# Optimization experiments

Hardware: AMD Instinct MI355X
Metric: run time of the kernel (lower is better)

The kernel has to match this reference:

```python
import jax, jax.numpy as jnp
import numpy as np

SELU_SCALE = 1.0507009873554805
SELU_ALPHA = 1.6732632423543772

def _learned_activation(x, w):
    # softmax-blended mixture of 8 activations plus a zero 'linear' branch
    p = jax.nn.softmax(w)
    sig = jax.nn.sigmoid(x)
    elu = jax.nn.elu(x)
    tanh = jnp.tanh(x)
    relu = jax.nn.relu(x)
    silu = jax.nn.silu(x)
    gelu = jax.nn.gelu(x, approximate=False)
    selu = SELU_SCALE * jnp.where(x > 0, x, SELU_ALPHA * jnp.expm1(x))
    mish = x * jnp.tanh(jax.nn.softplus(x))
    return (p[0] * sig + p[1] * elu + p[2] * tanh + p[3] * relu
            + p[4] * silu + p[5] * gelu + p[6] * selu + p[7] * mish)  # p[8]*0 (linear=0)


def setup_inputs() -> dict:
    key = jax.random.key(0)
    ks = jax.random.split(key, 10)
    B, D, H, E, M = 1024, 1024, 2048, 8, 2048
    init_units = 1024
    s = lambda fan_in: 1.0 / np.sqrt(fan_in)
    x = jax.random.normal(ks[0], (B, D), jnp.float32)
    gate_w = jax.random.normal(ks[1], (D, E), jnp.float32) * s(D)
    expert_w = jax.random.normal(ks[2], (E, D, H), jnp.float32) * s(D)
    expert_b = jnp.zeros((E, H), jnp.float32)
    conn_w1 = jax.random.normal(ks[3], (E, H, 32), jnp.float32) * s(H)
    conn_b1 = jnp.zeros((E, 32), jnp.float32)
    conn_w2 = jax.random.normal(ks[4], (E, 32, H), jnp.float32) * s(32)
    conn_b2 = jnp.zeros((E, H), jnp.float32)
    neuron_avg = jax.random.uniform(ks[5], (E, H), jnp.float32)
    # initial mask: first initial_units neurons active per expert
    neuron_mask = jnp.tile(
        jnp.concatenate([jnp.ones((init_units,), jnp.float32),
                         jnp.zeros((H - init_units,), jnp.float32)])[None, :], (E, 1))
    mem_read_w = jax.random.normal(ks[6], (H, M), jnp.float32) * s(H)
    mem_read_b = jnp.zeros((M,), jnp.float32)
    memory = jax.random.normal(ks[7], (M, H), jnp.float32) * s(M)
    act_w = jnp.ones((9,), jnp.float32)
    return {"x": x, "gate_w": gate_w, "expert_w": expert_w, "expert_b": expert_b,
            "conn_w1": conn_w1, "conn_b1": conn_b1, "conn_w2": conn_w2, "conn_b2": conn_b2,
            "neuron_avg": neuron_avg, "neuron_mask": neuron_mask,
            "mem_read_w": mem_read_w, "mem_read_b": mem_read_b,
            "memory": memory, "act_w": act_w}


def reference(x, gate_w, expert_w, expert_b, conn_w1, conn_b1, conn_w2, conn_b2,
              neuron_avg, neuron_mask, mem_read_w, mem_read_b, memory, act_w):
    # --- MoE gate over experts ---
    gate = jax.nn.softmax(x @ gate_w, axis=-1)  # [B, E]
    # --- DynamicConnectivity soft gating, per expert (from neuron_activation_avg) ---
    h1 = jax.nn.relu(jnp.einsum('eh,ehk->ek', neuron_avg, conn_w1) + conn_b1)  # [E, 32]
    conn = jax.nn.sigmoid(jnp.einsum('ek,ekh->eh', h1, conn_w2) + conn_b2)     # [E, H]
    # --- plastic dense experts: z -> gated -> masked -> relu ---
    z = jnp.einsum('bd,edh->ebh', x, expert_w) + expert_b[:, None, :]  # [E, B, H]
    a = jax.nn.relu(z * (conn * neuron_mask)[:, None, :])              # [E, B, H]
    moe_out = jnp.einsum('be,ebh->bh', gate, a)                        # [B, H]
    # --- episodic memory read (attention over memory slots) ---
    attn = jax.nn.softmax(moe_out @ mem_read_w + mem_read_b, axis=-1)  # [B, M]
    read_vec = attn @ memory                                           # [B, H]
    # --- blended learned activation on residual sum ---
    return _learned_activation(moe_out + read_vec, act_w)
```

## Files before the change

kernel.cpp:

```cpp
#include <hip/hip_runtime.h>
#include <hip/hip_bf16.h>
#include <math.h>

typedef __bf16 bf16_t;
typedef __bf16 bf16x8 __attribute__((ext_vector_type(8)));
typedef float f32x4 __attribute__((ext_vector_type(4)));

#define B_DIM 1024
#define D_DIM 1024
#define H_DIM 2048
#define E_DIM 8
#define M_DIM 2048

typedef const __attribute__((address_space(1))) unsigned int as1_uint;
typedef __attribute__((address_space(3))) unsigned int as3_uint;

__device__ __forceinline__ void gl_lds16(const void* g, void* l) {
  __builtin_amdgcn_global_load_lds((as1_uint*)g, (as3_uint*)l, 16, 0, 0);
}

__global__ __launch_bounds__(256) void cvt_kernel(const float* __restrict__ in,
                                                  bf16_t* __restrict__ out) {
  size_t i = ((size_t)blockIdx.x * 256 + threadIdx.x) * 8;
  float4 a = *(const float4*)&in[i];
  float4 b = *(const float4*)&in[i + 4];
  bf16x8 o;
  o[0] = (bf16_t)a.x; o[1] = (bf16_t)a.y; o[2] = (bf16_t)a.z; o[3] = (bf16_t)a.w;
  o[4] = (bf16_t)b.x; o[5] = (bf16_t)b.y; o[6] = (bf16_t)b.z; o[7] = (bf16_t)b.w;
  *(bf16x8*)&out[i] = o;
}

__global__ __launch_bounds__(256) void transpose_all(
    const float* __restrict__ ew, const float* __restrict__ mrw, const float* __restrict__ mem,
    bf16_t* __restrict__ wbT, bf16_t* __restrict__ mrT, bf16_t* __restrict__ memT) {
  __shared__ float tile[64][65];
  const int z = blockIdx.z;
  const float* in; bf16_t* out; int R, C;
  if (z < 8) {
    if (blockIdx.y >= 16) return;
    in = ew + (size_t)z * D_DIM * H_DIM; out = wbT + (size_t)z * D_DIM * H_DIM;
    R = D_DIM; C = H_DIM;
  } else if (z == 8) {
    in = mrw; out = mrT; R = H_DIM; C = M_DIM;
  } else {
    in = mem; out = memT; R = M_DIM; C = H_DIM;
  }
  int c0 = blockIdx.x * 64, r0 = blockIdx.y * 64;
  int t = threadIdx.x;
  int cq = (t & 15) * 4, rr = t >> 4;
#pragma unroll
  for (int i = 0; i < 4; ++i) {
    int r = rr + 16 * i;
    float4 v = *(const float4*)&in[(size_t)(r0 + r) * C + c0 + cq];
    tile[r][cq] = v.x; tile[r][cq + 1] = v.y; tile[r][cq + 2] = v.z; tile[r][cq + 3] = v.w;
  }
  __syncthreads();
  int r8 = (t & 7) * 8, cc = t >> 3;
#pragma unroll
  for (int i = 0; i < 2; ++i) {
    int c = cc + 32 * i;
    bf16x8 o;
#pragma unroll
    for (int j = 0; j < 8; ++j) o[j] = (bf16_t)tile[r8 + j][c];
    *(bf16x8*)&out[(size_t)(c0 + c) * R + r0 + r8] = o;
  }
}

__global__ __launch_bounds__(256) void gate_kernel(
    const float* __restrict__ x, const float* __restrict__ gw, float* __restrict__ gate_t) {
  __shared__ float red[256][8];
  int b = blockIdx.x, t = threadIdx.x;
  float acc[8] = {0.f, 0.f, 0.f, 0.f, 0.f, 0.f, 0.f, 0.f};
  for (int d = t; d < D_DIM; d += 256) {
    float xv = x[(size_t)b * D_DIM + d];
#pragma unroll
    for (int e = 0; e < 8; ++e) acc[e] += xv * gw[d * 8 + e];
  }
#pragma unroll
  for (int e = 0; e < 8; ++e) red[t][e] = acc[e];
  __syncthreads();
  for (int s = 128; s > 0; s >>= 1) {
    if (t < s) {
#pragma unroll
      for (int e = 0; e < 8; ++e) red[t][e] += red[t + s][e];
    }
    __syncthreads();
  }
  if (t == 0) {
    float m = red[0][0];
#pragma unroll
    for (int e = 1; e < 8; ++e) m = fmaxf(m, red[0][e]);
    float p[8], sum = 0.f;
#pragma unroll
    for (int e = 0; e < 8; ++e) { p[e] = expf(red[0][e] - m); sum += p[e]; }
    float inv = 1.f / sum;
#pragma unroll
    for (int e = 0; e < 8; ++e) gate_t[e * B_DIM + b] = p[e] * inv;
  }
}

__global__ __launch_bounds__(256) void conn1_kernel(
    const float* __restrict__ avg, const float* __restrict__ w1, float* __restrict__ h1p) {
  __shared__ float red[256 * 32];
  int e = blockIdx.x >> 3, c = blockIdx.x & 7, t = threadIdx.x;
  int h = c * 256 + t;
  float av = avg[e * H_DIM + h];
  const float* w1p = &w1[((size_t)e * H_DIM + h) * 32];
#pragma unroll
  for (int k = 0; k < 32; ++k) red[t * 32 + k] = av * w1p[k];
  __syncthreads();
  for (int s = 128; s > 0; s >>= 1) {
    if (t < s) {
#pragma unroll
      for (int k = 0; k < 32; ++k) red[t * 32 + k] += red[(t + s) * 32 + k];
    }
    __syncthreads();
  }
  if (t < 32) h1p[(e * 8 + c) * 32 + t] = red[t];
}

__global__ __launch_bounds__(256) void conn2_kernel(
    const float* __restrict__ h1p, const float* __restrict__ b1,
    const float* __restrict__ w2, const float* __restrict__ b2,
    const float* __restrict__ mask, float* __restrict__ conn) {
  __shared__ float h1[32];
  int e = blockIdx.x >> 3, c = blockIdx.x & 7, t = threadIdx.x;
  if (t < 32) {
    float s = 0.f;
#pragma unroll
    for (int c2 = 0; c2 < 8; ++c2) s += h1p[(e * 8 + c2) * 32 + t];
    h1[t] = fmaxf(s + b1[e * 32 + t], 0.f);
  }
  __syncthreads();
  int h = c * 256 + t;
  float s = b2[e * H_DIM + h];
#pragma unroll
  for (int k = 0; k < 32; ++k) s += h1[k] * w2[((size_t)e * 32 + k) * H_DIM + h];
  conn[e * H_DIM + h] = (1.f / (1.f + expf(-s))) * mask[e * H_DIM + h];
}

__global__ __launch_bounds__(512, 2) void expert_gemm(
    const bf16_t* __restrict__ A, const bf16_t* __restrict__ Bt,
    float* __restrict__ moe, bf16_t* __restrict__ moebf,
    const float* __restrict__ gate_t, const float* __restrict__ conn,
    const float* __restrict__ ebias) {
  __shared__ bf16_t As[2][128 * 64];
  __shared__ bf16_t Bs[8][64 * 64];

  const int wid = (blockIdx.x & 7) * 32 + (blockIdx.x >> 3);
  const int b0 = (wid & 7) * 128;
  const int n0 = (wid >> 3) * 64;

  const int t = threadIdx.x;
  const int lane = t & 63, wave = t >> 6;
  const int wmh = wave >> 2, wnq = wave & 3;
  const int lr = lane & 15, lk = (lane >> 4) * 8;
  const int csw = (lr & 7) << 3;
  const int srow = lane >> 3;
  const int scol = ((lane & 7) ^ srow) << 3;
  const size_t EB = (size_t)H_DIM * D_DIM;

  const bf16_t* Asrc = A + (size_t)(b0 + wave * 16 + srow) * D_DIM + scol;
  const bf16_t* Bsrc = Bt + (size_t)(n0 + wave * 8 + srow) * D_DIM + scol;

  auto stageA = [&](int buf, int kt) {
    gl_lds16(Asrc + (size_t)kt * 64, &As[buf][(wave * 16) * 64]);
    gl_lds16(Asrc + 8 * D_DIM + (size_t)kt * 64, &As[buf][(wave * 16 + 8) * 64]);
  };
  auto stageB = [&](int buf, int e, int kt) {
    gl_lds16(Bsrc + (size_t)e * EB + (size_t)kt * 64, &Bs[buf][(wave * 8) * 64]);
  };

  f32x4 acc[8][4];
#pragma unroll
  for (int e = 0; e < 8; ++e)
#pragma unroll
    for (int mf = 0; mf < 4; ++mf) acc[e][mf] = (f32x4){0.f, 0.f, 0.f, 0.f};

  stageA(0, 0);
#pragma unroll
  for (int s = 0; s < 5; ++s) stageB(s, s, 0);

  for (int kt = 0; kt < 16; ++kt) {
    const int ab = kt & 1;
    const bool nl = (kt < 15);
    bf16x8 af[2][4];
#pragma unroll
    for (int e = 0; e < 8; ++e) {
      if (e < 3) {
        stageB((e + 5) & 7, (e + 5) & 7, kt);
      } else if (nl) {
        stageB((e + 5) & 7, (e + 5) & 7, kt + 1);
        if (e == 3) stageA(ab ^ 1, kt + 1);
      }
      if (e < 3) {
        asm volatile("s_waitcnt vmcnt(5)" ::: "memory");
      } else if (nl) {
        asm volatile("s_waitcnt vmcnt(7)" ::: "memory");
      } else {
        if (e == 3) asm volatile("s_waitcnt vmcnt(4)" ::: "memory");
        if (e == 4) asm volatile("s_waitcnt vmcnt(3)" ::: "memory");
        if (e == 5) asm volatile("s_waitcnt vmcnt(2)" ::: "memory");
        if (e == 6) asm volatile("s_waitcnt vmcnt(1)" ::: "memory");
        if (e == 7) asm volatile("s_waitcnt vmcnt(0)" ::: "memory");
      }
      __builtin_amdgcn_s_barrier();
      __builtin_amdgcn_sched_barrier(0);
      if (e == 0) {
#pragma unroll
        for (int kk = 0; kk < 2; ++kk)
#pragma unroll
          for (int mf = 0; mf < 4; ++mf)
            af[kk][mf] = *(const bf16x8*)&As[ab][(wmh * 64 + mf * 16 + lr) * 64 +
                                                ((kk * 32 + lk) ^ csw)];
      }
      const bf16_t* Bb = &Bs[e][0];
      bf16x8 bf0 = *(const bf16x8*)&Bb[(wnq * 16 + lr) * 64 + (lk ^ csw)];
      bf16x8 bf1 = *(const bf16x8*)&Bb[(wnq * 16 + lr) * 64 + ((32 + lk) ^ csw)];
      __builtin_amdgcn_s_setprio(1);
#pragma unroll
      for (int mf = 0; mf < 4; ++mf) {
        acc[e][mf] = __builtin_amdgcn_mfma_f32_16x16x32_bf16(af[0][mf], bf0, acc[e][mf], 0, 0, 0);
        acc[e][mf] = __builtin_amdgcn_mfma_f32_16x16x32_bf16(af[1][mf], bf1, acc[e][mf], 0, 0, 0);
      }
      __builtin_amdgcn_s_setprio(0);
      __builtin_amdgcn_sched_barrier(0);
    }
  }

  const int r4 = (lane >> 4) * 4;
  const int gcol = n0 + wnq * 16 + lr;
  const int growb = b0 + wmh * 64;
  f32x4 sum[4];
#pragma unroll
  for (int mf = 0; mf < 4; ++mf) sum[mf] = (f32x4){0.f, 0.f, 0.f, 0.f};
#pragma unroll
  for (int e = 0; e < 8; ++e) {
    const float cm = conn[e * H_DIM + gcol];
    const float bb = ebias[e * H_DIM + gcol];
#pragma unroll
    for (int mf = 0; mf < 4; ++mf) {
      const float4 g4 = *(const float4*)&gate_t[e * B_DIM + growb + mf * 16 + r4];
      sum[mf][0] += fmaxf((acc[e][mf][0] + bb) * cm, 0.f) * g4.x;
      sum[mf][1] += fmaxf((acc[e][mf][1] + bb) * cm, 0.f) * g4.y;
      sum[mf][2] += fmaxf((acc[e][mf][2] + bb) * cm, 0.f) * g4.z;
      sum[mf][3] += fmaxf((acc[e][mf][3] + bb) * cm, 0.f) * g4.w;
    }
  }
#pragma unroll
  for (int mf = 0; mf < 4; ++mf)
#pragma unroll
    for (int j = 0; j < 4; ++j) {
      const int grow = growb + mf * 16 + r4 + j;
      moe[(size_t)grow * H_DIM + gcol] = sum[mf][j];
      moebf[(size_t)grow * H_DIM + gcol] = (bf16_t)sum[mf][j];
    }
}

__global__ __launch_bounds__(256, 2) void gemm_sk2(
    const bf16_t* __restrict__ A, const bf16_t* __restrict__ Bt, float* __restrict__ C) {
  __shared__ bf16_t As[2][128 * 64];
  __shared__ bf16_t Bs[2][128 * 64];

  const int wid = (blockIdx.x & 7) * 32 + (blockIdx.x >> 3);
  const int ez = wid >> 7;
  const int rem = wid & 127;
  const int b0 = (rem & 7) * 128;
  const int n0 = (rem >> 3) * 128;
  const int kbase = ez << 10;

  const int t = threadIdx.x;
  const int lane = t & 63, wave = t >> 6;
  const int wm = wave >> 1, wn = wave & 1;
  const int lr = lane & 15, lk = (lane >> 4) * 8;
  const int csw = (lr & 7) << 3;
  const int srow = lane >> 3;
  const int scol = ((lane & 7) ^ srow) << 3;

  const bf16_t* Arow = A + (size_t)(b0 + srow) * 2048 + kbase + scol;
  const bf16_t* Brow = Bt + (size_t)(n0 + srow) * 2048 + kbase + scol;

  const f32x4 zv = {0.f, 0.f, 0.f, 0.f};
  f32x4 acc[4][4];
#pragma unroll
  for (int mf = 0; mf < 4; ++mf)
#pragma unroll
    for (int nf = 0; nf < 4; ++nf) acc[mf][nf] = zv;

  auto STAGE = [&](int bsel, int kt) {
    const int ko = kt << 6;
#pragma unroll
    for (int i = 0; i < 4; ++i) {
      int rb = i * 32 + wave * 8;
      gl_lds16(Arow + (size_t)rb * 2048 + ko, &As[bsel][rb * 64]);
      gl_lds16(Brow + (size_t)rb * 2048 + ko, &Bs[bsel][rb * 64]);
    }
  };

  auto COMPUTE = [&](int bsel) {
    bf16x8 bfr[2][4];
#pragma unroll
    for (int kk = 0; kk < 2; ++kk)
#pragma unroll
      for (int nf = 0; nf < 4; ++nf)
        bfr[kk][nf] = *(const bf16x8*)&Bs[bsel][(wn * 64 + nf * 16 + lr) * 64 + ((kk * 32 + lk) ^ csw)];
    __builtin_amdgcn_s_setprio(1);
#pragma unroll
    for (int mf = 0; mf < 4; ++mf) {
      bf16x8 a0 = *(const bf16x8*)&As[bsel][(wm * 64 + mf * 16 + lr) * 64 + (lk ^ csw)];
      bf16x8 a1 = *(const bf16x8*)&As[bsel][(wm * 64 + mf * 16 + lr) * 64 + ((32 + lk) ^ csw)];
#pragma unroll
      for (int nf = 0; nf < 4; ++nf)
        acc[mf][nf] = __builtin_amdgcn_mfma_f32_16x16x32_bf16(a0, bfr[0][nf], acc[mf][nf], 0, 0, 0);
#pragma unroll
      for (int nf = 0; nf < 4; ++nf)
        acc[mf][nf] = __builtin_amdgcn_mfma_f32_16x16x32_bf16(a1, bfr[1][nf], acc[mf][nf], 0, 0, 0);
    }
    __builtin_amdgcn_s_setprio(0);
  };

  STAGE(0, 0);
  __syncthreads();
  for (int kt = 0; kt < 15; ++kt) {
    STAGE((kt + 1) & 1, kt + 1);
    COMPUTE(kt & 1);
    __syncthreads();
  }
  COMPUTE(1);

  const int r4 = (lane >> 4) * 4;
#pragma unroll
  for (int mf = 0; mf < 4; ++mf) {
#pragma unroll
    for (int nf = 0; nf < 4; ++nf) {
      int gcol = n0 + wn * 64 + nf * 16 + lr;
#pragma unroll
      for (int j = 0; j < 4; ++j) {
        int grow = b0 + wm * 64 + mf * 16 + r4 + j;
        C[((size_t)ez * B_DIM + grow) * 2048 + gcol] = acc[mf][nf][j];
      }
    }
  }
}

__global__ __launch_bounds__(256) void softmax_kernel(
    const float* __restrict__ lg, const float* __restrict__ bias, bf16_t* __restrict__ attn) {
  const size_t P = (size_t)B_DIM * M_DIM;
  int b = blockIdx.x, t = threadIdx.x;
  int lane = t & 63, wave = t >> 6;
  __shared__ float rmax[4], rsum[4];
  float v[8];
  float m = -1e30f;
#pragma unroll
  for (int i = 0; i < 8; ++i) {
    size_t idx = (size_t)b * M_DIM + i * 256 + t;
    v[i] = lg[idx] + lg[P + idx] + bias[i * 256 + t];
    m = fmaxf(m, v[i]);
  }
#pragma unroll
  for (int off = 32; off >= 1; off >>= 1) m = fmaxf(m, __shfl_xor(m, off));
  if (lane == 0) rmax[wave] = m;
  __syncthreads();
  m = fmaxf(fmaxf(rmax[0], rmax[1]), fmaxf(rmax[2], rmax[3]));
  float s = 0.f;
#pragma unroll
  for (int i = 0; i < 8; ++i) {
    v[i] = __expf(v[i] - m);
    s += v[i];
  }
#pragma unroll
  for (int off = 32; off >= 1; off >>= 1) s += __shfl_xor(s, off);
  if (lane == 0) rsum[wave] = s;
  __syncthreads();
  s = rsum[0] + rsum[1] + rsum[2] + rsum[3];
  float inv = 1.f / s;
#pragma unroll
  for (int i = 0; i < 8; ++i) attn[(size_t)b * M_DIM + i * 256 + t] = (bf16_t)(v[i] * inv);
}

__global__ __launch_bounds__(256) void act_kernel(
    const float* __restrict__ rdv, const float* __restrict__ aw, float* __restrict__ out) {
  const size_t P = (size_t)B_DIM * H_DIM;
  int i = blockIdx.x * 256 + threadIdx.x;
  float w[9], m = -1e30f;
#pragma unroll
  for (int j = 0; j < 9; ++j) { w[j] = aw[j]; m = fmaxf(m, w[j]); }
  float p[9], s = 0.f;
#pragma unroll
  for (int j = 0; j < 9; ++j) { p[j] = expf(w[j] - m); s += p[j]; }
  float inv = 1.f / s;
#pragma unroll
  for (int j = 0; j < 9; ++j) p[j] *= inv;
  float4 mv = ((const float4*)out)[i];
  float4 r0 = ((const float4*)rdv)[i];
  float4 r1 = ((const float4*)(rdv + P))[i];
  float xs[4] = {mv.x + r0.x + r1.x, mv.y + r0.y + r1.y,
                 mv.z + r0.z + r1.z, mv.w + r0.w + r1.w};
  float os[4];
#pragma unroll
  for (int q = 0; q < 4; ++q) {
    float xv = xs[q];
    float enx = expf(-xv);
    float ex = expf(xv);
    float sig = 1.f / (1.f + enx);
    float em1 = expm1f(xv);
    float th = tanhf(xv);
    float rl = fmaxf(xv, 0.f);
    float si = xv * sig;
    float ge = 0.5f * xv * (1.f + erff(xv * 0.70710678118654752f));
    float se = 1.0507009873554805f * (xv > 0.f ? xv : 1.6732632423543772f * em1);
    float el = xv > 0.f ? xv : em1;
    float sp = log1pf(ex);
    float mi = xv * tanhf(sp);
    os[q] = p[0] * sig + p[1] * el + p[2] * th + p[3] * rl + p[4] * si + p[5] * ge + p[6] * se + p[7] * mi;
  }
  ((float4*)out)[i] = make_float4(os[0], os[1], os[2], os[3]);
}

extern "C" void kernel_launch(void* const* d_in, const int* in_sizes, int n_in,
                              void* d_out, int out_size, void* d_ws, size_t ws_size,
                              hipStream_t stream) {
  const float* x        = (const float*)d_in[0];
  const float* gate_w   = (const float*)d_in[1];
  const float* expert_w = (const float*)d_in[2];
  const float* expert_b = (const float*)d_in[3];
  const float* conn_w1  = (const float*)d_in[4];
  const float* conn_b1  = (const float*)d_in[5];
  const float* conn_w2  = (const float*)d_in[6];
  const float* conn_b2  = (const float*)d_in[7];
  const float* navg     = (const float*)d_in[8];
  const float* nmask    = (const float*)d_in[9];
  const float* mem_rw   = (const float*)d_in[10];
  const float* mem_rb   = (const float*)d_in[11];
  const float* memory   = (const float*)d_in[12];
  const float* act_w    = (const float*)d_in[13];
  float* out = (float*)d_out;

  char* ws = (char*)d_ws;
  bf16_t* wbT    = (bf16_t*)(ws + 0);
  bf16_t* mrT    = (bf16_t*)(ws + 33554432);
  bf16_t* memT   = (bf16_t*)(ws + 41943040);
  float*  gate_t = (float*)(ws + 50331648);
  float*  connb  = (float*)(ws + 50364416);
  bf16_t* x_bf   = (bf16_t*)(ws + 50429952);
  bf16_t* moe_bf = (bf16_t*)(ws + 52527104);
  float*  h1p    = (float*)(ws + 56721408);
  float*  logits = (float*)(ws + 0);
  bf16_t* attn   = (bf16_t*)(ws + 16777216);
  float*  readv  = (float*)(ws + 0);
  float*  moe    = out;

  cvt_kernel<<<dim3(512), 256, 0, stream>>>(x, x_bf);
  transpose_all<<<dim3(32, 32, 10), 256, 0, stream>>>(expert_w, mem_rw, memory, wbT, mrT, memT);
  gate_kernel<<<dim3(B_DIM), 256, 0, stream>>>(x, gate_w, gate_t);
  conn1_kernel<<<dim3(64), 256, 0, stream>>>(navg, conn_w1, h1p);
  conn2_kernel<<<dim3(64), 256, 0, stream>>>(h1p, conn_b1, conn_w2, conn_b2, nmask, connb);
  expert_gemm<<<dim3(256), 512, 0, stream>>>(x_bf, wbT, moe, moe_bf, gate_t, connb, expert_b);
  gemm_sk2<<<dim3(256), 256, 0, stream>>>(moe_bf, mrT, logits);
  softmax_kernel<<<dim3(B_DIM), 256, 0, stream>>>(logits, mem_rb, attn);
  gemm_sk2<<<dim3(256), 256, 0, stream>>>(attn, memT, readv);
  act_kernel<<<dim3((B_DIM * H_DIM) / (256 * 4)), 256, 0, stream>>>(readv, act_w, out);
}
```

Before: 146.8 us.

## Prefetch B fragments across experts and double waves in split-K GEMM

In the expert GEMM, B-fragment LDS reads for the next expert are issued before the barrier so they overlap the current expert's MFMAs. The staging schedule is reordered so the A tile for the next k-step loads at the first expert, and the vmcnt waits are retuned to match. Separately, gemm_sk2 moves from 256 to 512 threads, so each wave computes a 64x32 sub-tile instead of 64x64, for more waves per tile and fewer accumulator registers. The risks are higher LDS read traffic per MFMA in gemm_sk2 and subtle ordering hazards in the retuned wait counts.

```diff
diff --git a/kernel.cpp b/kernel.cpp
--- a/kernel.cpp
+++ b/kernel.cpp
@@ -18,6 +18,8 @@
 __device__ __forceinline__ void gl_lds16(const void* g, void* l) {
   __builtin_amdgcn_global_load_lds((as1_uint*)g, (as3_uint*)l, 16, 0, 0);
 }
+
+#define WAITV(n) asm volatile("s_waitcnt vmcnt(" #n ")" ::: "memory")
 
 __global__ __launch_bounds__(256) void cvt_kernel(const float* __restrict__ in,
                                                   bf16_t* __restrict__ out) {
@@ -167,9 +169,14 @@
     gl_lds16(Asrc + (size_t)kt * 64, &As[buf][(wave * 16) * 64]);
     gl_lds16(Asrc + 8 * D_DIM + (size_t)kt * 64, &As[buf][(wave * 16 + 8) * 64]);
   };
-  auto stageB = [&](int buf, int e, int kt) {
-    gl_lds16(Bsrc + (size_t)e * EB + (size_t)kt * 64, &Bs[buf][(wave * 8) * 64]);
+  auto stageB = [&](int slot, int e, int kt) {
+    gl_lds16(Bsrc + (size_t)e * EB + (size_t)kt * 64, &Bs[slot][(wave * 8) * 64]);
   };
+  auto readB = [&](int slot, bf16x8& r0, bf16x8& r1) {
+    const bf16_t* Bb = &Bs[slot][0];
+    r0 = *(const bf16x8*)&Bb[(wnq * 16 + lr) * 64 + (lk ^ csw)];
+    r1 = *(const bf16x8*)&Bb[(wnq * 16 + lr) * 64 + ((32 + lk) ^ csw)];
+  };
 
   f32x4 acc[8][4];
 #pragma unroll
@@ -180,29 +187,32 @@
   stageA(0, 0);
 #pragma unroll
   for (int s = 0; s < 5; ++s) stageB(s, s, 0);
+  WAITV(3);
+  __builtin_amdgcn_s_barrier();
+  __builtin_amdgcn_sched_barrier(0);
+  bf16x8 bc0, bc1, bn0, bn1;
+  readB(0, bc0, bc1);
 
   for (int kt = 0; kt < 16; ++kt) {
     const int ab = kt & 1;
-    const bool nl = (kt < 15);
+    const bool last = (kt == 15);
     bf16x8 af[2][4];
 #pragma unroll
     for (int e = 0; e < 8; ++e) {
+      if (!(last && e == 7)) readB((e + 1) & 7, bn0, bn1);
       if (e < 3) {
-        stageB((e + 5) & 7, (e + 5) & 7, kt);
-      } else if (nl) {
-        stageB((e + 5) & 7, (e + 5) & 7, kt + 1);
-        if (e == 3) stageA(ab ^ 1, kt + 1);
+        stageB((e + 5) & 7, e + 5, kt);
+        if (e == 0 && !last) stageA(ab ^ 1, kt + 1);
+      } else if (!last) {
+        stageB((e + 5) & 7, e - 3, kt + 1);
       }
-      if (e < 3) {
-        asm volatile("s_waitcnt vmcnt(5)" ::: "memory");
-      } else if (nl) {
-        asm volatile("s_waitcnt vmcnt(7)" ::: "memory");
+      if (!last) {
+        if (e < 4) { WAITV(5); } else { WAITV(3); }
       } else {
-        if (e == 3) asm volatile("s_waitcnt vmcnt(4)" ::: "memory");
-        if (e == 4) asm volatile("s_waitcnt vmcnt(3)" ::: "memory");
-        if (e == 5) asm volatile("s_waitcnt vmcnt(2)" ::: "memory");
-        if (e == 6) asm volatile("s_waitcnt vmcnt(1)" ::: "memory");
-        if (e == 7) asm volatile("s_waitcnt vmcnt(0)" ::: "memory");
+        if (e < 3)       { WAITV(3); }
+        else if (e == 3) { WAITV(2); }
+        else if (e == 4) { WAITV(1); }
+        else             { WAITV(0); }
       }
       __builtin_amdgcn_s_barrier();
       __builtin_amdgcn_sched_barrier(0);
@@ -214,17 +224,14 @@
             af[kk][mf] = *(const bf16x8*)&As[ab][(wmh * 64 + mf * 16 + lr) * 64 +
                                                 ((kk * 32 + lk) ^ csw)];
       }
-      const bf16_t* Bb = &Bs[e][0];
-      bf16x8 bf0 = *(const bf16x8*)&Bb[(wnq * 16 + lr) * 64 + (lk ^ csw)];
-      bf16x8 bf1 = *(const bf16x8*)&Bb[(wnq * 16 + lr) * 64 + ((32 + lk) ^ csw)];
       __builtin_amdgcn_s_setprio(1);
 #pragma unroll
       for (int mf = 0; mf < 4; ++mf) {
-        acc[e][mf] = __builtin_amdgcn_mfma_f32_16x16x32_bf16(af[0][mf], bf0, acc[e][mf], 0, 0, 0);
-        acc[e][mf] = __builtin_amdgcn_mfma_f32_16x16x32_bf16(af[1][mf], bf1, acc[e][mf], 0, 0, 0);
+        acc[e][mf] = __builtin_amdgcn_mfma_f32_16x16x32_bf16(af[0][mf], bc0, acc[e][mf], 0, 0, 0);
+        acc[e][mf] = __builtin_amdgcn_mfma_f32_16x16x32_bf16(af[1][mf], bc1, acc[e][mf], 0, 0, 0);
       }
       __builtin_amdgcn_s_setprio(0);
-      __builtin_amdgcn_sched_barrier(0);
+      bc0 = bn0; bc1 = bn1;
     }
   }
 
@@ -257,7 +264,7 @@
     }
 }
 
-__global__ __launch_bounds__(256, 2) void gemm_sk2(
+__global__ __launch_bounds__(512, 2) void gemm_sk2(
     const bf16_t* __restrict__ A, const bf16_t* __restrict__ Bt, float* __restrict__ C) {
   __shared__ bf16_t As[2][128 * 64];
   __shared__ bf16_t Bs[2][128 * 64];
@@ -271,7 +278,7 @@
 
   const int t = threadIdx.x;
   const int lane = t & 63, wave = t >> 6;
-  const int wm = wave >> 1, wn = wave & 1;
+  const int wm = wave >> 2, wn = wave & 3;
   const int lr = lane & 15, lk = (lane >> 4) * 8;
   const int csw = (lr & 7) << 3;
   const int srow = lane >> 3;
@@ -281,39 +288,39 @@
   const bf16_t* Brow = Bt + (size_t)(n0 + srow) * 2048 + kbase + scol;
 
   const f32x4 zv = {0.f, 0.f, 0.f, 0.f};
-  f32x4 acc[4][4];
+  f32x4 acc[4][2];
 #pragma unroll
   for (int mf = 0; mf < 4; ++mf)
 #pragma unroll
-    for (int nf = 0; nf < 4; ++nf) acc[mf][nf] = zv;
+    for (int nf = 0; nf < 2; ++nf) acc[mf][nf] = zv;
 
   auto STAGE = [&](int bsel, int kt) {
     const int ko = kt << 6;
 #pragma unroll
-    for (int i = 0; i < 4; ++i) {
-      int rb = i * 32 + wave * 8;
+    for (int i = 0; i < 2; ++i) {
+      int rb = i * 64 + wave * 8;
       gl_lds16(Arow + (size_t)rb * 2048 + ko, &As[bsel][rb * 64]);
       gl_lds16(Brow + (size_t)rb * 2048 + ko, &Bs[bsel][rb * 64]);
     }
   };
 
   auto COMPUTE = [&](int bsel) {
-    bf16x8 bfr[2][4];
+    bf16x8 bfr[2][2];
 #pragma unroll
     for (int kk = 0; kk < 2; ++kk)
 #pragma unroll
-      for (int nf = 0; nf < 4; ++nf)
-        bfr[kk][nf] = *(const bf16x8*)&Bs[bsel][(wn * 64 + nf * 16 + lr) * 64 + ((kk * 32 + lk) ^ csw)];
+      for (int nf = 0; nf < 2; ++nf)
+        bfr[kk][nf] = *(const bf16x8*)&Bs[bsel][(wn * 32 + nf * 16 + lr) * 64 + ((kk * 32 + lk) ^ csw)];
     __builtin_amdgcn_s_setprio(1);
 #pragma unroll
     for (int mf = 0; mf < 4; ++mf) {
       bf16x8 a0 = *(const bf16x8*)&As[bsel][(wm * 64 + mf * 16 + lr) * 64 + (lk ^ csw)];
       bf16x8 a1 = *(const bf16x8*)&As[bsel][(wm * 64 + mf * 16 + lr) * 64 + ((32 + lk) ^ csw)];
 #pragma unroll
-      for (int nf = 0; nf < 4; ++nf)
+      for (int nf = 0; nf < 2; ++nf)
         acc[mf][nf] = __builtin_amdgcn_mfma_f32_16x16x32_bf16(a0, bfr[0][nf], acc[mf][nf], 0, 0, 0);
 #pragma unroll
-      for (int nf = 0; nf < 4; ++nf)
+      for (int nf = 0; nf < 2; ++nf)
         acc[mf][nf] = __builtin_amdgcn_mfma_f32_16x16x32_bf16(a1, bfr[1][nf], acc[mf][nf], 0, 0, 0);
     }
     __builtin_amdgcn_s_setprio(0);
@@ -332,8 +339,8 @@
 #pragma unroll
   for (int mf = 0; mf < 4; ++mf) {
 #pragma unroll
-    for (int nf = 0; nf < 4; ++nf) {
-      int gcol = n0 + wn * 64 + nf * 16 + lr;
+    for (int nf = 0; nf < 2; ++nf) {
+      int gcol = n0 + wn * 32 + nf * 16 + lr;
 #pragma unroll
       for (int j = 0; j < 4; ++j) {
         int grow = b0 + wm * 64 + mf * 16 + r4 + j;
@@ -456,8 +463,8 @@
   conn1_kernel<<<dim3(64), 256, 0, stream>>>(navg, conn_w1, h1p);
   conn2_kernel<<<dim3(64), 256, 0, stream>>>(h1p, conn_b1, conn_w2, conn_b2, nmask, connb);
   expert_gemm<<<dim3(256), 512, 0, stream>>>(x_bf, wbT, moe, moe_bf, gate_t, connb, expert_b);
-  gemm_sk2<<<dim3(256), 256, 0, stream>>>(moe_bf, mrT, logits);
+  gemm_sk2<<<dim3(256), 512, 0, stream>>>(moe_bf, mrT, logits);
   softmax_kernel<<<dim3(B_DIM), 256, 0, stream>>>(logits, mem_rb, attn);
-  gemm_sk2<<<dim3(256), 256, 0, stream>>>(attn, memT, readv);
+  gemm_sk2<<<dim3(256), 512, 0, stream>>>(attn, memT, readv);
   act_kernel<<<dim3((B_DIM * H_DIM) / (256 * 4)), 256, 0, stream>>>(readv, act_w, out);
 }
```

Measured after the change: 140.0 us. 4.7% less time.
